# Performance work log

Hardware: AMD Instinct MI355X
Metric: run time of the kernel (lower is better)

## Reference

```python
import jax, jax.numpy as jnp
import numpy as np
from jax import lax

BATCH, HID = 8192, 512


def setup_inputs() -> dict:
    key = jax.random.key(0)
    ks = jax.random.split(key, 9)
    s = 0.05
    return {
        "h": jax.random.normal(ks[0], (BATCH, HID), jnp.float32),
        "W1": jax.random.normal(ks[1], (2 * HID, HID), jnp.float32) * s,
        "b1": jax.random.normal(ks[2], (2 * HID,), jnp.float32) * s,
        "W2": jax.random.normal(ks[3], (2 * HID, 2 * HID), jnp.float32) * s,
        "b2": jax.random.normal(ks[4], (2 * HID,), jnp.float32) * s,
        "W3": jax.random.normal(ks[5], (HID, 2 * HID), jnp.float32) * s,
        "b3": jax.random.normal(ks[6], (HID,), jnp.float32) * s,
        "Wt": jax.random.normal(ks[7], (HID, 1), jnp.float32) * s,
        "bt": jax.random.normal(ks[8], (HID,), jnp.float32) * s,
        "n_steps": 10,
    }


def reference(h, W1, b1, W2, b2, W3, b3, Wt, bt, n_steps):
    dt = 1.0 / n_steps  # t_span = (0, 1)

    def ode_func(t, hh):
        # time_embed(Linear(1,H)) on a column of t's: t * Wt[:,0] + bt
        t_emb = t * Wt[:, 0] + bt                      # (H,), broadcast over batch
        x = hh + t_emb                                 # (B, H)
        x = jnp.tanh(x @ W1.T + b1)                    # (B, 2H)
        x = jnp.tanh(x @ W2.T + b2)                    # (B, 2H)
        return x @ W3.T + b3                           # (B, H)

    def rk4_step(hh, t):
        k1 = ode_func(t, hh)
        k2 = ode_func(t + dt / 2, hh + dt / 2 * k1)
        k3 = ode_func(t + dt / 2, hh + dt / 2 * k2)
        k4 = ode_func(t + dt, hh + dt * k3)
        return hh + dt / 6 * (k1 + 2 * k2 + 2 * k3 + k4), None

    ts = (jnp.arange(n_steps, dtype=h.dtype) * dt)     # step start times
    h_out, _ = lax.scan(rk4_step, h, ts)
    return h_out
```

## Files before the change

### kernel.cpp

```cpp
#include <hip/hip_runtime.h>
#include <hip/hip_bf16.h>
#include <math.h>
#include <stdint.h>

using bf16 = __hip_bfloat16;
typedef __attribute__((ext_vector_type(8))) short short8;
typedef __attribute__((ext_vector_type(4))) float floatx4;
typedef __attribute__((ext_vector_type(4))) int int4v;

typedef const __attribute__((address_space(1))) void* gptr_t;
typedef __attribute__((address_space(3))) void* lptr_t;

__device__ __forceinline__ void load_lds16(const void* g, void* l) {
    __builtin_amdgcn_global_load_lds((gptr_t)(uintptr_t)g, (lptr_t)(uintptr_t)l, 16, 0, 0);
}

#define WAIT_VM(n) __builtin_amdgcn_s_waitcnt(0x0F70 | ((n) & 15) | (((n) >> 4) << 14))

__device__ __forceinline__ float fast_tanh(float x) {
    float e = __expf(2.f * x);
    return 1.f - 2.f / (e + 1.f);
}


template <int K, int N>
__global__ void __launch_bounds__(256, 2)
gemm_tanh4(const bf16* __restrict__ A, const bf16* __restrict__ W,
           const float* __restrict__ bias, int8_t* __restrict__ out) {
    constexpr int MT = 4, NT = 4;
    constexpr int nIter = K / 64;
    __shared__ alignas(16) bf16 lA[2][128 * 64];
    __shared__ alignas(16) bf16 lB[2][128 * 64];

    const int b   = blockIdx.x + gridDim.x * blockIdx.y;
    const int xcd = b & 7, j = b >> 3;
    const int bx  = j & 7;
    const int by  = xcd + 8 * (j >> 3);

    const int tid  = threadIdx.x;
    const int lane = tid & 63;
    const int w    = tid >> 6;
    const int wr   = w >> 1, wc = w & 1;
    const int quad = lane >> 4, l16 = lane & 15;
    const int brow = by * 128;
    const int bcol = bx * 128;

    const bf16* gA[4]; const bf16* gW[4]; int lq[4];
#pragma unroll
    for (int jj = 0; jj < 4; ++jj) {
        const int q = tid + jj * 256;
        const int r = q >> 3, s = (q & 7) ^ (r & 7);
        gA[jj] = A + (size_t)(brow + r) * K + s * 8;
        gW[jj] = W + (size_t)(bcol + r) * K + s * 8;
        lq[jj] = q * 8;
    }

    floatx4 acc[MT][NT];
    const floatx4 zero = {0.f, 0.f, 0.f, 0.f};
#pragma unroll
    for (int mt = 0; mt < MT; ++mt)
#pragma unroll
        for (int nt = 0; nt < NT; ++nt) acc[mt][nt] = zero;

    const int arow0 = wr * 64 + l16;
    const int brow0 = wc * 64 + l16;
    const int x7 = l16 & 7;

#pragma unroll
    for (int jj = 0; jj < 4; ++jj) load_lds16(gA[jj], &lA[0][0] + lq[jj]);
#pragma unroll
    for (int jj = 0; jj < 4; ++jj) load_lds16(gW[jj], &lB[0][0] + lq[jj]);

#pragma unroll
    for (int kt = 0; kt < nIter; ++kt) {
        constexpr int dummy = 0; (void)dummy;
        const int cur = kt & 1;
        if (kt + 1 < nIter) {
#pragma unroll
            for (int jj = 0; jj < 4; ++jj)
                load_lds16(gA[jj] + (kt + 1) * 64, &lA[cur ^ 1][0] + lq[jj]);
#pragma unroll
            for (int jj = 0; jj < 4; ++jj)
                load_lds16(gW[jj] + (kt + 1) * 64, &lB[cur ^ 1][0] + lq[jj]);
            WAIT_VM(8);
        } else {
            WAIT_VM(0);
        }
        __builtin_amdgcn_s_barrier();

#pragma unroll
        for (int kk = 0; kk < 2; ++kk) {
            const int sw = ((kk * 4 + quad) ^ x7) * 8;
            short8 af[MT], bfr[NT];
#pragma unroll
            for (int mt = 0; mt < MT; ++mt)
                af[mt] = *(const short8*)(&lA[cur][0] + (arow0 + mt * 16) * 64 + sw);
#pragma unroll
            for (int nt = 0; nt < NT; ++nt)
                bfr[nt] = *(const short8*)(&lB[cur][0] + (brow0 + nt * 16) * 64 + sw);
#pragma unroll
            for (int mt = 0; mt < MT; ++mt)
#pragma unroll
                for (int nt = 0; nt < NT; ++nt)
                    acc[mt][nt] = __builtin_amdgcn_mfma_f32_16x16x32_bf16(
                        af[mt], bfr[nt], acc[mt][nt], 0, 0, 0);
        }
        __builtin_amdgcn_s_barrier();
    }

    const int m0 = brow + wr * 64 + quad * 4;
    const int n0 = bcol + wc * 64 + l16;
#pragma unroll
    for (int mt = 0; mt < MT; ++mt)
#pragma unroll
        for (int nt = 0; nt < NT; ++nt) {
            const int n = n0 + nt * 16;
            const float bb = bias[n];
#pragma unroll
            for (int i = 0; i < 4; ++i) {
                const int m = m0 + mt * 16 + i;
                const float t = fast_tanh(acc[mt][nt][i] + bb);
                out[(size_t)m * N + n] = (int8_t)__float2int_rn(t * 127.f);
            }
        }
}

template <int K, int N>
__global__ void __launch_bounds__(256, 2)
gemm_tanh_i8(const int8_t* __restrict__ A, const int8_t* __restrict__ W,
             const float* __restrict__ dq, const float* __restrict__ bias,
             int8_t* __restrict__ out) {
    constexpr int MT = 4, NT = 4;
    constexpr int nIter = K / 128;
    __shared__ alignas(16) int8_t lA[2][128 * 128];
    __shared__ alignas(16) int8_t lB[2][128 * 128];

    const int b   = blockIdx.x + gridDim.x * blockIdx.y;
    const int xcd = b & 7, j = b >> 3;
    const int bx  = j & 7;
    const int by  = xcd + 8 * (j >> 3);

    const int tid  = threadIdx.x;
    const int lane = tid & 63;
    const int w    = tid >> 6;
    const int wr   = w >> 1, wc = w & 1;
    const int quad = lane >> 4, l16 = lane & 15;
    const int brow = by * 128;
    const int bcol = bx * 128;

    const int8_t* gA[4]; const int8_t* gW[4]; int lq[4];
#pragma unroll
    for (int jj = 0; jj < 4; ++jj) {
        const int q = tid + jj * 256;
        const int r = q >> 3, s = (q & 7) ^ (r & 7);
        gA[jj] = A + (size_t)(brow + r) * K + s * 16;
        gW[jj] = W + (size_t)(bcol + r) * K + s * 16;
        lq[jj] = q * 16;
    }

    int4v acc[MT][NT];
    const int4v izero = {0, 0, 0, 0};
#pragma unroll
    for (int mt = 0; mt < MT; ++mt)
#pragma unroll
        for (int nt = 0; nt < NT; ++nt) acc[mt][nt] = izero;

    const int arow0 = wr * 64 + l16;
    const int brow0 = wc * 64 + l16;
    const int x7 = l16 & 7;

#pragma unroll
    for (int jj = 0; jj < 4; ++jj) load_lds16(gA[jj], &lA[0][0] + lq[jj]);
#pragma unroll
    for (int jj = 0; jj < 4; ++jj) load_lds16(gW[jj], &lB[0][0] + lq[jj]);

#pragma unroll
    for (int kt = 0; kt < nIter; ++kt) {
        const int cur = kt & 1;
        if (kt + 1 < nIter) {
#pragma unroll
            for (int jj = 0; jj < 4; ++jj)
                load_lds16(gA[jj] + (kt + 1) * 128, &lA[cur ^ 1][0] + lq[jj]);
#pragma unroll
            for (int jj = 0; jj < 4; ++jj)
                load_lds16(gW[jj] + (kt + 1) * 128, &lB[cur ^ 1][0] + lq[jj]);
            WAIT_VM(8);
        } else {
            WAIT_VM(0);
        }
        __builtin_amdgcn_s_barrier();

#pragma unroll
        for (int kk = 0; kk < 2; ++kk) {
            const int sw = ((kk * 4 + quad) ^ x7) * 16;
            int4v af[MT], bfr[NT];
#pragma unroll
            for (int mt = 0; mt < MT; ++mt)
                af[mt] = *(const int4v*)(&lA[cur][(arow0 + mt * 16) * 128 + sw]);
#pragma unroll
            for (int nt = 0; nt < NT; ++nt)
                bfr[nt] = *(const int4v*)(&lB[cur][(brow0 + nt * 16) * 128 + sw]);
#pragma unroll
            for (int mt = 0; mt < MT; ++mt)
#pragma unroll
                for (int nt = 0; nt < NT; ++nt)
                    acc[mt][nt] = __builtin_amdgcn_mfma_i32_16x16x64_i8(
                        af[mt], bfr[nt], acc[mt][nt], 0, 0, 0);
        }
        __builtin_amdgcn_s_barrier();
    }

    const int m0 = brow + wr * 64 + quad * 4;
    const int n0 = bcol + wc * 64 + l16;
#pragma unroll
    for (int mt = 0; mt < MT; ++mt)
#pragma unroll
        for (int nt = 0; nt < NT; ++nt) {
            const int n = n0 + nt * 16;
            const float bb = bias[n];
            const float dqn = dq[n];
#pragma unroll
            for (int i = 0; i < 4; ++i) {
                const int m = m0 + mt * 16 + i;
                const float t = fast_tanh((float)acc[mt][nt][i] * dqn + bb);
                out[(size_t)m * N + n] = (int8_t)__float2int_rn(t * 127.f);
            }
        }
}

template <int MODE, bool HASX0>
__global__ void __launch_bounds__(256, 2)
gemm_k(const int8_t* __restrict__ A, const int8_t* __restrict__ W,
       const float* __restrict__ dq, const float* __restrict__ bias,
       bf16* __restrict__ kacc, const bf16* __restrict__ hb_src,
       const float* __restrict__ h_src, float* __restrict__ h_out,
       bf16* __restrict__ hb_out, bf16* __restrict__ x0_out,
       const float* __restrict__ temb, float alpha, float dt6) {
    constexpr int MT = 4, NT = 2, K = 1024;
    constexpr int nIter = K / 128;
    __shared__ alignas(16) int8_t lA[2][128 * 128];
    __shared__ alignas(16) int8_t lB[2][64 * 128];

    const int b   = blockIdx.x + gridDim.x * blockIdx.y;
    const int xcd = b & 7, j = b >> 3;
    const int bx  = j & 7;
    const int by  = xcd + 8 * (j >> 3);

    const int tid  = threadIdx.x;
    const int lane = tid & 63;
    const int w    = tid >> 6;
    const int wr   = w >> 1, wc = w & 1;
    const int quad = lane >> 4, l16 = lane & 15;
    const int brow = by * 128;
    const int bcol = bx * 64;

    const int8_t* gA[4]; int lqA[4];
    const int8_t* gW[2]; int lqB[2];
#pragma unroll
    for (int jj = 0; jj < 4; ++jj) {
        const int q = tid + jj * 256;
        const int r = q >> 3, s = (q & 7) ^ (r & 7);
        gA[jj]  = A + (size_t)(brow + r) * K + s * 16;
        lqA[jj] = q * 16;
    }
#pragma unroll
    for (int jj = 0; jj < 2; ++jj) {
        const int q = tid + jj * 256;
        const int r = q >> 3, s = (q & 7) ^ (r & 7);
        gW[jj]  = W + (size_t)(bcol + r) * K + s * 16;
        lqB[jj] = q * 16;
    }

    int4v acc[MT][NT];
    const int4v izero = {0, 0, 0, 0};
#pragma unroll
    for (int mt = 0; mt < MT; ++mt)
#pragma unroll
        for (int nt = 0; nt < NT; ++nt) acc[mt][nt] = izero;

    const int arow0 = wr * 64 + l16;
    const int brow0 = wc * 32 + l16;
    const int x7 = l16 & 7;

#pragma unroll
    for (int jj = 0; jj < 4; ++jj) load_lds16(gA[jj], &lA[0][0] + lqA[jj]);
#pragma unroll
    for (int jj = 0; jj < 2; ++jj) load_lds16(gW[jj], &lB[0][0] + lqB[jj]);

#pragma unroll
    for (int kt = 0; kt < nIter; ++kt) {
        const int cur = kt & 1;
        if (kt + 1 < nIter) {
#pragma unroll
            for (int jj = 0; jj < 4; ++jj)
                load_lds16(gA[jj] + (kt + 1) * 128, &lA[cur ^ 1][0] + lqA[jj]);
#pragma unroll
            for (int jj = 0; jj < 2; ++jj)
                load_lds16(gW[jj] + (kt + 1) * 128, &lB[cur ^ 1][0] + lqB[jj]);
            WAIT_VM(6);
        } else {
            WAIT_VM(0);
        }
        __builtin_amdgcn_s_barrier();

#pragma unroll
        for (int kk = 0; kk < 2; ++kk) {
            const int sw = ((kk * 4 + quad) ^ x7) * 16;
            int4v af[MT], bfr[NT];
#pragma unroll
            for (int mt = 0; mt < MT; ++mt)
                af[mt] = *(const int4v*)(&lA[cur][(arow0 + mt * 16) * 128 + sw]);
#pragma unroll
            for (int nt = 0; nt < NT; ++nt)
                bfr[nt] = *(const int4v*)(&lB[cur][(brow0 + nt * 16) * 128 + sw]);
#pragma unroll
            for (int mt = 0; mt < MT; ++mt)
#pragma unroll
                for (int nt = 0; nt < NT; ++nt)
                    acc[mt][nt] = __builtin_amdgcn_mfma_i32_16x16x64_i8(
                        af[mt], bfr[nt], acc[mt][nt], 0, 0, 0);
        }
        __builtin_amdgcn_s_barrier();
    }

    const int m0 = brow + wr * 64 + quad * 4;
    const int n0 = bcol + wc * 32 + l16;
#pragma unroll
    for (int mt = 0; mt < MT; ++mt)
#pragma unroll
        for (int nt = 0; nt < NT; ++nt) {
            const int n = n0 + nt * 16;
            const float bb = bias[n];
            const float dqn = dq[n];
            const float te = temb[n];
#pragma unroll
            for (int i = 0; i < 4; ++i) {
                const int m = m0 + mt * 16 + i;
                const size_t idx = (size_t)m * 512 + n;
                const float kv = (float)acc[mt][nt][i] * dqn + bb;
                if constexpr (MODE == 0) {
                    kacc[idx] = __float2bfloat16(kv);
                    x0_out[idx] = __float2bfloat16(
                        __bfloat162float(hb_src[idx]) + alpha * kv + te);
                } else if constexpr (MODE == 1) {
                    kacc[idx] = __float2bfloat16(__bfloat162float(kacc[idx]) + 2.f * kv);
                    x0_out[idx] = __float2bfloat16(
                        __bfloat162float(hb_src[idx]) + alpha * kv + te);
                } else {
                    const float hn = h_src[idx] + dt6 * (__bfloat162float(kacc[idx]) + kv);
                    h_out[idx] = hn;
                    hb_out[idx] = __float2bfloat16(hn);
                    if constexpr (HASX0) x0_out[idx] = __float2bfloat16(hn + te);
                }
            }
        }
}

__global__ void f2b_kern(const float* __restrict__ src, bf16* __restrict__ dst, int n) {
    const int i = blockIdx.x * blockDim.x + threadIdx.x;
    if (i < n) dst[i] = __float2bfloat16(src[i]);
}

__global__ void quantW_row(const float* __restrict__ W, int K,
                           int8_t* __restrict__ out, float* __restrict__ dq) {
    __shared__ float red[256];
    const int row = blockIdx.x, tid = threadIdx.x;
    const float* src = W + (size_t)row * K;
    float m = 0.f;
    for (int k = tid; k < K; k += 256) m = fmaxf(m, fabsf(src[k]));
    red[tid] = m;
    __syncthreads();
    for (int s = 128; s > 0; s >>= 1) {
        if (tid < s) red[tid] = fmaxf(red[tid], red[tid + s]);
        __syncthreads();
    }
    const float rmax = fmaxf(red[0], 1e-8f);
    const float sc = 127.f / rmax;
    int8_t* dst = out + (size_t)row * K;
    for (int k = tid; k < K; k += 256) {
        int v = __float2int_rn(src[k] * sc);
        v = v > 127 ? 127 : (v < -127 ? -127 : v);
        dst[k] = (int8_t)v;
    }
    if (tid == 0) dq[row] = rmax / (127.f * 127.f);
}

__global__ void prep_kern(const float* __restrict__ h, const float* __restrict__ bt,
                          const float* __restrict__ Wt, float* __restrict__ temb,
                          bf16* __restrict__ x0, bf16* __restrict__ hb,
                          float half_dt, int total) {
    const int i = blockIdx.x * blockDim.x + threadIdx.x;
    if (i < total) {
        const float hv = h[i];
        x0[i] = __float2bfloat16(hv + bt[i & 511]);
        hb[i] = __float2bfloat16(hv);
    }
    if (i < 21 * 512) {
        const int jj = i >> 9, n = i & 511;
        temb[i] = (jj * half_dt) * Wt[n] + bt[n];
    }
}

extern "C" void kernel_launch(void* const* d_in, const int* in_sizes, int n_in,
                              void* d_out, int out_size, void* d_ws, size_t ws_size,
                              hipStream_t stream) {
    const float* h_in = (const float*)d_in[0];
    const float* W1 = (const float*)d_in[1];
    const float* b1 = (const float*)d_in[2];
    const float* W2 = (const float*)d_in[3];
    const float* b2 = (const float*)d_in[4];
    const float* W3 = (const float*)d_in[5];
    const float* b3 = (const float*)d_in[6];
    const float* Wt = (const float*)d_in[7];
    const float* bt = (const float*)d_in[8];
    const int B = 8192, H = 512, H2 = 1024, NS = 10;
    const float dt = 1.f / NS;

    char* ws = (char*)d_ws;
    auto alloc = [&](size_t bytes) {
        char* p = ws;
        ws += (bytes + 255) & ~(size_t)255;
        return p;
    };
    bf16* W1b = (bf16*)alloc((size_t)H2 * H * 2);
    int8_t* W2i = (int8_t*)alloc((size_t)H2 * H2);
    float* dq2  = (float*)alloc((size_t)H2 * 4);
    int8_t* W3i = (int8_t*)alloc((size_t)H * H2);
    float* dq3  = (float*)alloc((size_t)H * 4);
    bf16* x0b = (bf16*)alloc((size_t)B * H * 2);
    int8_t* x1i = (int8_t*)alloc((size_t)B * H2);
    int8_t* x2i = (int8_t*)alloc((size_t)B * H2);
    bf16* kacc = (bf16*)alloc((size_t)B * H * 2);
    bf16* hb   = (bf16*)alloc((size_t)B * H * 2);
    float* temb = (float*)alloc((size_t)21 * H * 4);
    float* hbuf = (float*)d_out;

    {
        int n = H2 * H;
        f2b_kern<<<(n + 255) / 256, 256, 0, stream>>>(W1, W1b, n);
        quantW_row<<<H2, 256, 0, stream>>>(W2, H2, W2i, dq2);
        quantW_row<<<H, 256, 0, stream>>>(W3, H2, W3i, dq3);
    }
    {
        const int total = B * H;
        prep_kern<<<(total + 255) / 256, 256, 0, stream>>>(
            h_in, bt, Wt, temb, x0b, hb, dt * 0.5f, total);
    }

    const dim3 blk256(256);
    const dim3 g12(H2 / 128, B / 128);
    const dim3 g3(H / 64, B / 128);

    for (int s = 0; s < NS; ++s) {
        const float* hs = (s == 0) ? h_in : hbuf;
        const float* tmid = temb + (size_t)(2 * s + 1) * H;
        const float* tend = temb + (size_t)(2 * s + 2) * H;
        for (int e = 0; e < 4; ++e) {
            gemm_tanh4<512, 1024><<<g12, blk256, 0, stream>>>(x0b, W1b, b1, x1i);
            gemm_tanh_i8<1024, 1024><<<g12, blk256, 0, stream>>>(x1i, W2i, dq2, b2, x2i);
            if (e == 0)
                gemm_k<0, true><<<g3, blk256, 0, stream>>>(
                    x2i, W3i, dq3, b3, kacc, hb, hs, nullptr, nullptr, x0b,
                    tmid, dt * 0.5f, 0.f);
            else if (e == 1)
                gemm_k<1, true><<<g3, blk256, 0, stream>>>(
                    x2i, W3i, dq3, b3, kacc, hb, hs, nullptr, nullptr, x0b,
                    tmid, dt * 0.5f, 0.f);
            else if (e == 2)
                gemm_k<1, true><<<g3, blk256, 0, stream>>>(
                    x2i, W3i, dq3, b3, kacc, hb, hs, nullptr, nullptr, x0b,
                    tend, dt, 0.f);
            else if (s != NS - 1)
                gemm_k<2, true><<<g3, blk256, 0, stream>>>(
                    x2i, W3i, dq3, b3, kacc, hb, hs, hbuf, hb, x0b,
                    tend, 0.f, dt / 6.f);
            else
                gemm_k<2, false><<<g3, blk256, 0, stream>>>(
                    x2i, W3i, dq3, b3, kacc, hb, hs, hbuf, hb, nullptr,
                    tend, 0.f, dt / 6.f);
        }
    }
}
```

Baseline: 1.771 ms.

## Quantize first-layer GEMM to int8 with dynamic per-step activation scale

```diff
diff --git a/kernel.cpp b/kernel.cpp
--- a/kernel.cpp
+++ b/kernel.cpp
@@ -22,15 +22,26 @@
     return 1.f - 2.f / (e + 1.f);
 }
 
+__device__ __forceinline__ int8_t q_i8(float x, float inv127S) {
+    int v = __float2int_rn(x * inv127S);
+    v = v > 127 ? 127 : (v < -127 ? -127 : v);
+    return (int8_t)v;
+}
+
+__device__ __forceinline__ void atomicMaxPosF(float* p, float v) {
+    atomicMax(reinterpret_cast<int*>(p), __float_as_int(v));
+}
+
 
 template <int K, int N>
 __global__ void __launch_bounds__(256, 2)
-gemm_tanh4(const bf16* __restrict__ A, const bf16* __restrict__ W,
-           const float* __restrict__ bias, int8_t* __restrict__ out) {
+gemm_l1(const int8_t* __restrict__ A, const int8_t* __restrict__ W,
+        const float* __restrict__ dq, const float* __restrict__ bias,
+        int8_t* __restrict__ out, float* __restrict__ slots) {
     constexpr int MT = 4, NT = 4;
-    constexpr int nIter = K / 64;
-    __shared__ alignas(16) bf16 lA[2][128 * 64];
-    __shared__ alignas(16) bf16 lB[2][128 * 64];
+    constexpr int nIter = K / 128;
+    __shared__ alignas(16) int8_t lA[2][128 * 128];
+    __shared__ alignas(16) int8_t lB[2][128 * 128];
 
     const int b   = blockIdx.x + gridDim.x * blockIdx.y;
     const int xcd = b & 7, j = b >> 3;
@@ -38,6 +49,13 @@
     const int by  = xcd + 8 * (j >> 3);
 
     const int tid  = threadIdx.x;
+
+    if (b == 0 && tid == 0) {
+        const float p = slots[1];
+        if (p > 0.f) { slots[0] = p; slots[1] = 0.f; }
+    }
+    const float xs = slots[2];
+
     const int lane = tid & 63;
     const int w    = tid >> 6;
     const int wr   = w >> 1, wc = w & 1;
@@ -45,22 +63,22 @@
     const int brow = by * 128;
     const int bcol = bx * 128;
 
-    const bf16* gA[4]; const bf16* gW[4]; int lq[4];
+    const int8_t* gA[4]; const int8_t* gW[4]; int lq[4];
 #pragma unroll
     for (int jj = 0; jj < 4; ++jj) {
         const int q = tid + jj * 256;
         const int r = q >> 3, s = (q & 7) ^ (r & 7);
-        gA[jj] = A + (size_t)(brow + r) * K + s * 8;
-        gW[jj] = W + (size_t)(bcol + r) * K + s * 8;
-        lq[jj] = q * 8;
-    }
-
-    floatx4 acc[MT][NT];
-    const floatx4 zero = {0.f, 0.f, 0.f, 0.f};
+        gA[jj] = A + (size_t)(brow + r) * K + s * 16;
+        gW[jj] = W + (size_t)(bcol + r) * K + s * 16;
+        lq[jj] = q * 16;
+    }
+
+    int4v acc[MT][NT];
+    const int4v izero = {0, 0, 0, 0};
 #pragma unroll
     for (int mt = 0; mt < MT; ++mt)
 #pragma unroll
-        for (int nt = 0; nt < NT; ++nt) acc[mt][nt] = zero;
+        for (int nt = 0; nt < NT; ++nt) acc[mt][nt] = izero;
 
     const int arow0 = wr * 64 + l16;
     const int brow0 = wc * 64 + l16;
@@ -73,15 +91,14 @@
 
 #pragma unroll
     for (int kt = 0; kt < nIter; ++kt) {
-        constexpr int dummy = 0; (void)dummy;
         const int cur = kt & 1;
         if (kt + 1 < nIter) {
 #pragma unroll
             for (int jj = 0; jj < 4; ++jj)
-                load_lds16(gA[jj] + (kt + 1) * 64, &lA[cur ^ 1][0] + lq[jj]);
+                load_lds16(gA[jj] + (kt + 1) * 128, &lA[cur ^ 1][0] + lq[jj]);
 #pragma unroll
             for (int jj = 0; jj < 4; ++jj)
-                load_lds16(gW[jj] + (kt + 1) * 64, &lB[cur ^ 1][0] + lq[jj]);
+                load_lds16(gW[jj] + (kt + 1) * 128, &lB[cur ^ 1][0] + lq[jj]);
             WAIT_VM(8);
         } else {
             WAIT_VM(0);
@@ -90,19 +107,19 @@
 
 #pragma unroll
         for (int kk = 0; kk < 2; ++kk) {
-            const int sw = ((kk * 4 + quad) ^ x7) * 8;
-            short8 af[MT], bfr[NT];
+            const int sw = ((kk * 4 + quad) ^ x7) * 16;
+            int4v af[MT], bfr[NT];
 #pragma unroll
             for (int mt = 0; mt < MT; ++mt)
-                af[mt] = *(const short8*)(&lA[cur][0] + (arow0 + mt * 16) * 64 + sw);
+                af[mt] = *(const int4v*)(&lA[cur][(arow0 + mt * 16) * 128 + sw]);
 #pragma unroll
             for (int nt = 0; nt < NT; ++nt)
-                bfr[nt] = *(const short8*)(&lB[cur][0] + (brow0 + nt * 16) * 64 + sw);
+                bfr[nt] = *(const int4v*)(&lB[cur][(brow0 + nt * 16) * 128 + sw]);
 #pragma unroll
             for (int mt = 0; mt < MT; ++mt)
 #pragma unroll
                 for (int nt = 0; nt < NT; ++nt)
-                    acc[mt][nt] = __builtin_amdgcn_mfma_f32_16x16x32_bf16(
+                    acc[mt][nt] = __builtin_amdgcn_mfma_i32_16x16x64_i8(
                         af[mt], bfr[nt], acc[mt][nt], 0, 0, 0);
         }
         __builtin_amdgcn_s_barrier();
@@ -116,10 +133,11 @@
         for (int nt = 0; nt < NT; ++nt) {
             const int n = n0 + nt * 16;
             const float bb = bias[n];
+            const float dqs = dq[n] * xs;
 #pragma unroll
             for (int i = 0; i < 4; ++i) {
                 const int m = m0 + mt * 16 + i;
-                const float t = fast_tanh(acc[mt][nt][i] + bb);
+                const float t = fast_tanh((float)acc[mt][nt][i] * dqs + bb);
                 out[(size_t)m * N + n] = (int8_t)__float2int_rn(t * 127.f);
             }
         }
@@ -234,8 +252,9 @@
        const float* __restrict__ dq, const float* __restrict__ bias,
        bf16* __restrict__ kacc, const bf16* __restrict__ hb_src,
        const float* __restrict__ h_src, float* __restrict__ h_out,
-       bf16* __restrict__ hb_out, bf16* __restrict__ x0_out,
-       const float* __restrict__ temb, float alpha, float dt6) {
+       bf16* __restrict__ hb_out, int8_t* __restrict__ x0_out,
+       const float* __restrict__ temb, float alpha, float dt6,
+       float* __restrict__ slots) {
     constexpr int MT = 4, NT = 2, K = 1024;
     constexpr int nIter = K / 128;
     __shared__ alignas(16) int8_t lA[2][128 * 128];
@@ -247,6 +266,10 @@
     const int by  = xcd + 8 * (j >> 3);
 
     const int tid  = threadIdx.x;
+    const float S    = slots[0] + 1.0f;
+    const float invS = 127.f / S;
+    if (HASX0 && b == 0 && tid == 0) slots[2] = S;
+
     const int lane = tid & 63;
     const int w    = tid >> 6;
     const int wr   = w >> 1, wc = w & 1;
@@ -325,6 +348,7 @@
 
     const int m0 = brow + wr * 64 + quad * 4;
     const int n0 = bcol + wc * 32 + l16;
+    float hmx = 0.f;
 #pragma unroll
     for (int mt = 0; mt < MT; ++mt)
 #pragma unroll
@@ -340,25 +364,46 @@
                 const float kv = (float)acc[mt][nt][i] * dqn + bb;
                 if constexpr (MODE == 0) {
                     kacc[idx] = __float2bfloat16(kv);
-                    x0_out[idx] = __float2bfloat16(
-                        __bfloat162float(hb_src[idx]) + alpha * kv + te);
+                    x0_out[idx] = q_i8(
+                        __bfloat162float(hb_src[idx]) + alpha * kv + te, invS);
                 } else if constexpr (MODE == 1) {
                     kacc[idx] = __float2bfloat16(__bfloat162float(kacc[idx]) + 2.f * kv);
-                    x0_out[idx] = __float2bfloat16(
-                        __bfloat162float(hb_src[idx]) + alpha * kv + te);
+                    x0_out[idx] = q_i8(
+                        __bfloat162float(hb_src[idx]) + alpha * kv + te, invS);
                 } else {
                     const float hn = h_src[idx] + dt6 * (__bfloat162float(kacc[idx]) + kv);
                     h_out[idx] = hn;
                     hb_out[idx] = __float2bfloat16(hn);
-                    if constexpr (HASX0) x0_out[idx] = __float2bfloat16(hn + te);
+                    if constexpr (HASX0) {
+                        x0_out[idx] = q_i8(hn + te, invS);
+                        hmx = fmaxf(hmx, fabsf(hn));
+                    }
                 }
             }
         }
-}
-
-__global__ void f2b_kern(const float* __restrict__ src, bf16* __restrict__ dst, int n) {
-    const int i = blockIdx.x * blockDim.x + threadIdx.x;
-    if (i < n) dst[i] = __float2bfloat16(src[i]);
+    if constexpr (MODE == 2 && HASX0) {
+#pragma unroll
+        for (int off = 32; off > 0; off >>= 1)
+            hmx = fmaxf(hmx, __shfl_down(hmx, off));
+        if (lane == 0) atomicMaxPosF(&slots[1], hmx);
+    }
+}
+
+
+__global__ void init_slots(float* __restrict__ slots) {
+    slots[0] = 0.f; slots[1] = 0.f; slots[2] = 1.f;
+}
+
+__global__ void hmax_kern(const float* __restrict__ h, int total,
+                          float* __restrict__ slots) {
+    const int stride = gridDim.x * blockDim.x;
+    float m = 0.f;
+    for (int i = blockIdx.x * blockDim.x + threadIdx.x; i < total; i += stride)
+        m = fmaxf(m, fabsf(h[i]));
+#pragma unroll
+    for (int off = 32; off > 0; off >>= 1)
+        m = fmaxf(m, __shfl_down(m, off));
+    if ((threadIdx.x & 63) == 0) atomicMaxPosF(&slots[0], m);
 }
 
 __global__ void quantW_row(const float* __restrict__ W, int K,
@@ -387,12 +432,15 @@
 
 __global__ void prep_kern(const float* __restrict__ h, const float* __restrict__ bt,
                           const float* __restrict__ Wt, float* __restrict__ temb,
-                          bf16* __restrict__ x0, bf16* __restrict__ hb,
-                          float half_dt, int total) {
+                          int8_t* __restrict__ x0q, bf16* __restrict__ hb,
+                          float half_dt, int total, float* __restrict__ slots) {
     const int i = blockIdx.x * blockDim.x + threadIdx.x;
+    const float S0 = slots[0] + 0.4f;
+    if (i == 0) { slots[2] = S0; slots[1] = 0.f; }
+    const float invS = 127.f / S0;
     if (i < total) {
         const float hv = h[i];
-        x0[i] = __float2bfloat16(hv + bt[i & 511]);
+        x0q[i] = q_i8(hv + bt[i & 511], invS);
         hb[i] = __float2bfloat16(hv);
     }
     if (i < 21 * 512) {
@@ -422,29 +470,32 @@
         ws += (bytes + 255) & ~(size_t)255;
         return p;
     };
-    bf16* W1b = (bf16*)alloc((size_t)H2 * H * 2);
+    int8_t* W1i = (int8_t*)alloc((size_t)H2 * H);
+    float* dq1  = (float*)alloc((size_t)H2 * 4);
     int8_t* W2i = (int8_t*)alloc((size_t)H2 * H2);
     float* dq2  = (float*)alloc((size_t)H2 * 4);
     int8_t* W3i = (int8_t*)alloc((size_t)H * H2);
     float* dq3  = (float*)alloc((size_t)H * 4);
-    bf16* x0b = (bf16*)alloc((size_t)B * H * 2);
+    int8_t* x0q = (int8_t*)alloc((size_t)B * H);
     int8_t* x1i = (int8_t*)alloc((size_t)B * H2);
     int8_t* x2i = (int8_t*)alloc((size_t)B * H2);
     bf16* kacc = (bf16*)alloc((size_t)B * H * 2);
     bf16* hb   = (bf16*)alloc((size_t)B * H * 2);
     float* temb = (float*)alloc((size_t)21 * H * 4);
+    float* slots = (float*)alloc(256);
     float* hbuf = (float*)d_out;
 
     {
-        int n = H2 * H;
-        f2b_kern<<<(n + 255) / 256, 256, 0, stream>>>(W1, W1b, n);
+        init_slots<<<1, 1, 0, stream>>>(slots);
+        hmax_kern<<<1024, 256, 0, stream>>>(h_in, B * H, slots);
+        quantW_row<<<H2, 256, 0, stream>>>(W1, H, W1i, dq1);
         quantW_row<<<H2, 256, 0, stream>>>(W2, H2, W2i, dq2);
         quantW_row<<<H, 256, 0, stream>>>(W3, H2, W3i, dq3);
     }
     {
         const int total = B * H;
         prep_kern<<<(total + 255) / 256, 256, 0, stream>>>(
-            h_in, bt, Wt, temb, x0b, hb, dt * 0.5f, total);
+            h_in, bt, Wt, temb, x0q, hb, dt * 0.5f, total, slots);
     }
 
     const dim3 blk256(256);
@@ -456,28 +507,30 @@
         const float* tmid = temb + (size_t)(2 * s + 1) * H;
         const float* tend = temb + (size_t)(2 * s + 2) * H;
         for (int e = 0; e < 4; ++e) {
-            gemm_tanh4<512, 1024><<<g12, blk256, 0, stream>>>(x0b, W1b, b1, x1i);
-            gemm_tanh_i8<1024, 1024><<<g12, blk256, 0, stream>>>(x1i, W2i, dq2, b2, x2i);
+            gemm_l1<512, 1024><<<g12, blk256, 0, stream>>>(x0q, W1i, dq1, b1,
+                                                           x1i, slots);
+            gemm_tanh_i8<1024, 1024><<<g12, blk256, 0, stream>>>(x1i, W2i, dq2,
+                                                                 b2, x2i);
             if (e == 0)
                 gemm_k<0, true><<<g3, blk256, 0, stream>>>(
-                    x2i, W3i, dq3, b3, kacc, hb, hs, nullptr, nullptr, x0b,
-                    tmid, dt * 0.5f, 0.f);
+                    x2i, W3i, dq3, b3, kacc, hb, hs, nullptr, nullptr, x0q,
+                    tmid, dt * 0.5f, 0.f, slots);
             else if (e == 1)
                 gemm_k<1, true><<<g3, blk256, 0, stream>>>(
-                    x2i, W3i, dq3, b3, kacc, hb, hs, nullptr, nullptr, x0b,
-                    tmid, dt * 0.5f, 0.f);
+                    x2i, W3i, dq3, b3, kacc, hb, hs, nullptr, nullptr, x0q,
+                    tmid, dt * 0.5f, 0.f, slots);
             else if (e == 2)
                 gemm_k<1, true><<<g3, blk256, 0, stream>>>(
-                    x2i, W3i, dq3, b3, kacc, hb, hs, nullptr, nullptr, x0b,
-                    tend, dt, 0.f);
+                    x2i, W3i, dq3, b3, kacc, hb, hs, nullptr, nullptr, x0q,
+                    tend, dt, 0.f, slots);
             else if (s != NS - 1)
                 gemm_k<2, true><<<g3, blk256, 0, stream>>>(
-                    x2i, W3i, dq3, b3, kacc, hb, hs, hbuf, hb, x0b,
-                    tend, 0.f, dt / 6.f);
+                    x2i, W3i, dq3, b3, kacc, hb, hs, hbuf, hb, x0q,
+                    tend, 0.f, dt / 6.f, slots);
             else
                 gemm_k<2, false><<<g3, blk256, 0, stream>>>(
                     x2i, W3i, dq3, b3, kacc, hb, hs, hbuf, hb, nullptr,
-                    tend, 0.f, dt / 6.f);
-        }
-    }
-}
+                    tend, 0.f, dt / 6.f, slots);
+        }
+    }
+}
```

Result: slower. 1.880 ms (+6.1%).
